# Kernel optimization log

Hardware: AMD Instinct MI355X
Metric: run time of the kernel (lower is better)

The kernel has to match this reference:

```python
import jax, jax.numpy as jnp
import numpy as np

D_MODEL = 1024
N_HEADS = 16
D_K = 64  # per-head dim and the scaling denominator used by the module
NEG = -1e9  # stand-in for -inf in masked_fill (rows are never fully masked)


def setup_inputs() -> dict:
    key = jax.random.key(0)
    ks = jax.random.split(key, 8)
    B, M, N = 2, 2048, 2048
    q = jax.random.normal(ks[0], (B, M, D_MODEL), dtype=jnp.float32)
    k = jax.random.normal(ks[1], (B, N, D_MODEL), dtype=jnp.float32)
    v = jax.random.normal(ks[2], (B, N, D_MODEL), dtype=jnp.float32)
    mask = jax.random.randint(ks[3], (B, M, N), 0, 2).astype(jnp.bool_)
    # xavier_uniform for square [d,d] weights: limit = sqrt(6/(d+d))
    lim = float(np.sqrt(6.0 / (D_MODEL + D_MODEL)))
    Wq = jax.random.uniform(ks[4], (D_MODEL, D_MODEL), jnp.float32, -lim, lim)
    Wk = jax.random.uniform(ks[5], (D_MODEL, D_MODEL), jnp.float32, -lim, lim)
    Wv = jax.random.uniform(ks[6], (D_MODEL, D_MODEL), jnp.float32, -lim, lim)
    Wo = jax.random.uniform(ks[7], (D_MODEL, D_MODEL), jnp.float32, -lim, lim)
    return {"q": q, "k": k, "v": v, "mask": mask,
            "Wq": Wq, "Wk": Wk, "Wv": Wv, "Wo": Wo}


def _split_heads(x):
    # (B, S, D) -> (B, H, S, Dh); the torch split/cat-on-batch trick is
    # mathematically identical to this standard head reshape.
    B, S, _ = x.shape
    return x.reshape(B, S, N_HEADS, D_K).transpose(0, 2, 1, 3)


def reference(q, k, v, mask, Wq, Wk, Wv, Wo):
    qw = _split_heads(q @ Wq.T)  # (B,H,M,Dh)
    kw = _split_heads(k @ Wk.T)  # (B,H,N,Dh)
    vw = _split_heads(v @ Wv.T)  # (B,H,N,Dh)
    scores = jnp.einsum('bhmd,bhnd->bhmn', qw, kw)
    scores = jnp.where(mask[:, None, :, :], NEG, scores)
    attn = jax.nn.softmax(scores / jnp.sqrt(jnp.float32(D_K)), axis=-1)
    ctx = jnp.einsum('bhmn,bhnd->bhmd', attn, vw)
    B, _, M, _ = ctx.shape
    ctx = ctx.transpose(0, 2, 1, 3).reshape(B, M, D_MODEL)
    return ctx @ Wo.T
```

## Files before the change

### kernel.cpp

```cpp
#include <hip/hip_runtime.h>
#include <hip/hip_bf16.h>
#include <stdint.h>
#include <string.h>

#define SEQ   2048
#define DM    1024
#define NH    16
#define NB    2

typedef __attribute__((ext_vector_type(8))) short bf16x8;
typedef __attribute__((ext_vector_type(4))) float f32x4;
typedef unsigned short u16;
typedef unsigned int   u32;

__device__ __forceinline__ u16 f2bf(float f) {
    u32 u = __float_as_uint(f);
    u += 0x7FFF + ((u >> 16) & 1);
    return (u16)(u >> 16);
}
__device__ __forceinline__ u32 pk2bf(float a, float b) {
    __hip_bfloat162 p = __float22bfloat162_rn(make_float2(a, b));
    u32 u; memcpy(&u, &p, 4); return u;
}
__device__ __forceinline__ float fexp2(float x) {
#if __has_builtin(__builtin_amdgcn_exp2f)
    return __builtin_amdgcn_exp2f(x);
#else
    return exp2f(x);
#endif
}
__device__ __forceinline__ float mask_exp2(float s, u32 lsel, int pos) {
#if __has_builtin(__builtin_amdgcn_sbfe)
    u32 keep = (u32)__builtin_amdgcn_sbfe((int)lsel, pos, 1);
#else
    u32 keep = (u32)((int)(lsel << (31 - pos)) >> 31);
#endif
    return __uint_as_float(__float_as_uint(fexp2(s)) & keep);
}
__device__ __forceinline__ void gl_lds16(const void* g, void* l) {
    __builtin_amdgcn_global_load_lds(
        (const __attribute__((address_space(1))) u32*)g,
        (__attribute__((address_space(3))) u32*)l, 16, 0, 0);
}
__device__ __forceinline__ void wbar_vm3() { asm volatile("s_waitcnt vmcnt(3)\ns_barrier" ::: "memory"); }
__device__ __forceinline__ void wbar_vm4() { asm volatile("s_waitcnt vmcnt(4)\ns_barrier" ::: "memory"); }
__device__ __forceinline__ void vm_drain() { asm volatile("s_waitcnt vmcnt(0)" ::: "memory"); }

struct CvtArgs {
    const float* s[7];
    u16* d[7];
    float scale[7];
    int start[8];
};
__global__ __launch_bounds__(256) void cvt_kernel(CvtArgs a) {
    int bid = blockIdx.x;
    int seg = 0;
#pragma unroll
    for (int i = 1; i < 7; ++i) if (bid >= a.start[i]) seg = i;
    float sc = a.scale[seg];
    size_t base = (size_t)(bid - a.start[seg]) * 2048 + threadIdx.x * 8;
    const float4* s4 = (const float4*)(a.s[seg] + base);
    float4 x = s4[0], y = s4[1];
    u32 r[4];
    r[0] = pk2bf(x.x*sc, x.y*sc); r[1] = pk2bf(x.z*sc, x.w*sc);
    r[2] = pk2bf(y.x*sc, y.y*sc); r[3] = pk2bf(y.z*sc, y.w*sc);
    *(uint4*)(a.d[seg] + base) = *(uint4*)r;
}

__global__ void maskpack_kernel(const int* __restrict__ mask,
                                unsigned int* __restrict__ bits) {
    int gid = blockIdx.x * 256 + threadIdx.x;
    int m = mask[gid];
    unsigned long long bal = __ballot(m != 0);
    int lane = threadIdx.x & 63;
    if (lane == 0)       bits[gid >> 5] = (u32)(bal & 0xFFFFFFFFull);
    else if (lane == 32) bits[gid >> 5] = (u32)(bal >> 32);
}

template<int RT>
__device__ __forceinline__ void gemm_body(const u16* __restrict__ A,
                                          const u16* __restrict__ Bm,
                                          void* __restrict__ Y,
                                          int rtile, int ctile, int mode,
                                          u16* sA, u16* sB) {
    constexpr int ABUF = RT * 32 * 32;
    constexpr int BBUF = 128 * 32;
    const int tid  = threadIdx.x;
    const int wv   = tid >> 6, lane = tid & 63;
    const int quad = lane >> 4, ln = lane & 15;
    const int wr   = wv >> 1,  wc  = wv & 1;

    const int lr4 = lane >> 2;
    const int lcc = ((lane & 3) ^ ((lane >> 3) & 3)) * 8;

    const u16* gA[RT/2]; u16* lA[RT/2];
#pragma unroll
    for (int s = 0; s < RT/2; ++s) {
        int seg = wv * (RT/2) + s;
        gA[s] = A + (size_t)(rtile * (RT*32) + seg*16 + lr4) * 1024 + lcc;
        lA[s] = sA + seg * 512;
    }
    const u16* gB[2]; u16* lB[2];
#pragma unroll
    for (int s = 0; s < 2; ++s) {
        int seg = wv * 2 + s;
        gB[s] = Bm + (size_t)(ctile * 128 + seg*16 + lr4) * 1024 + lcc;
        lB[s] = sB + seg * 512;
    }

    f32x4 acc[RT][4];
#pragma unroll
    for (int i = 0; i < RT; ++i)
#pragma unroll
        for (int j = 0; j < 4; ++j) acc[i][j] = (f32x4){0.f,0.f,0.f,0.f};

    const int c0 = (quad ^ ((ln >> 1) & 3)) * 8;

#pragma unroll
    for (int s = 0; s < RT/2; ++s) gl_lds16(gA[s], lA[s]);
#pragma unroll
    for (int s = 0; s < 2; ++s)    gl_lds16(gB[s], lB[s]);
#pragma unroll
    for (int s = 0; s < RT/2; ++s) gl_lds16(gA[s] + 32, lA[s] + ABUF);
#pragma unroll
    for (int s = 0; s < 2; ++s)    gl_lds16(gB[s] + 32, lB[s] + BBUF);

    int bc = 0, bp = 2;
    for (int kt = 0; kt < 32; ++kt) {
        if (RT == 4) wbar_vm4(); else wbar_vm3();
        int pk = (kt + 2) & 31;
#pragma unroll
        for (int s = 0; s < RT/2; ++s) gl_lds16(gA[s] + pk*32, lA[s] + bp*ABUF);
#pragma unroll
        for (int s = 0; s < 2; ++s)    gl_lds16(gB[s] + pk*32, lB[s] + bp*BBUF);

        const u16* sAb = sA + bc * ABUF;
        const u16* sBb = sB + bc * BBUF;
        bf16x8 af[RT], bfr[4];
#pragma unroll
        for (int rt = 0; rt < RT; ++rt)
            af[rt] = *(const bf16x8*)(sAb + (wr*(RT*16) + rt*16 + ln) * 32 + c0);
#pragma unroll
        for (int ct = 0; ct < 4; ++ct)
            bfr[ct] = *(const bf16x8*)(sBb + (wc*64 + ct*16 + ln) * 32 + c0);
#pragma unroll
        for (int rt = 0; rt < RT; ++rt)
#pragma unroll
            for (int ct = 0; ct < 4; ++ct)
                acc[rt][ct] = __builtin_amdgcn_mfma_f32_16x16x32_bf16(
                    af[rt], bfr[ct], acc[rt][ct], 0, 0, 0);

        bc = (bc == 2) ? 0 : bc + 1;
        bp = (bp == 2) ? 0 : bp + 1;
    }
    vm_drain();

#pragma unroll
    for (int rt = 0; rt < RT; ++rt) {
#pragma unroll
        for (int ct = 0; ct < 4; ++ct) {
#pragma unroll
            for (int i = 0; i < 4; ++i) {
                int R = rtile*(RT*32) + wr*(RT*16) + rt*16 + quad*4 + i;
                int C = ctile*128 + wc*64 + ct*16 + ln;
                float val = acc[rt][ct][i];
                if (mode == 0) {
                    int b = R >> 11, s = R & 2047, h = C >> 6, d = C & 63;
                    ((u16*)Y)[((size_t)((b*NH + h) * SEQ + s) << 6) + d] = f2bf(val);
                } else if (mode == 1) {
                    int h = R >> 6, d = R & 63, b = C >> 11, n = C & 2047;
                    ((u16*)Y)[((size_t)((b*NH + h) * 64 + d) << 11) + n] = f2bf(val);
                } else {
                    ((float*)Y)[(size_t)R * 1024 + C] = val;
                }
            }
        }
    }
}

struct QKVArgs { const u16* A[3]; const u16* B[3]; u16* Y[3]; };

__global__ __launch_bounds__(256) void gemm_qkv(QKVArgs g) {
    __shared__ u16 sA[3 * 128 * 32];
    __shared__ u16 sB[3 * 128 * 32];
    int z = blockIdx.z;
    if (z == 2)
        gemm_body<4>(g.A[2], g.B[2], g.Y[2], blockIdx.y, blockIdx.x, 1, sA, sB);
    else
        gemm_body<4>(g.A[z], g.B[z], g.Y[z], blockIdx.x, blockIdx.y, 0, sA, sB);
}

__global__ __launch_bounds__(256) void gemm_out(const u16* __restrict__ A,
                                                const u16* __restrict__ Bm,
                                                float* __restrict__ Y) {
    __shared__ u16 sA[3 * 64 * 32];
    __shared__ u16 sB[3 * 128 * 32];
    gemm_body<2>(A, Bm, Y, blockIdx.x, blockIdx.y, 2, sA, sB);
}

__global__ __launch_bounds__(512) void attn_kernel(
    const u16* __restrict__ qw,
    const u16* __restrict__ kw,
    const u16* __restrict__ vt,
    const u32* __restrict__ mbits,
    u16* __restrict__ ctx) {

    constexpr int RSD = 36;
    __shared__ u16 sK[3 * 4096];
    __shared__ u16 sV[3 * 4096];
    __shared__ u32 sPd[8 * 16 * RSD];

    const int mtile = blockIdx.x;
    const int bh    = blockIdx.y;
    const int b     = bh >> 4;
    const int tid   = threadIdx.x;
    const int wv    = tid >> 6, lane = tid & 63;
    const int quad  = lane >> 4, ln = lane & 15;
    const int m0    = mtile * 128;

    const size_t hbase = (size_t)bh * SEQ * 64;

    bf16x8 qf[2];
    {
        const u16* qp = qw + hbase + (size_t)(m0 + wv*16 + ln) * 64 + quad*8;
        qf[0] = *(const bf16x8*)(qp);
        qf[1] = *(const bf16x8*)(qp + 32);
    }

    f32x4 o[4], lsum;
    lsum = (f32x4){0.f,0.f,0.f,0.f};
#pragma unroll
    for (int j = 0; j < 4; ++j) o[j] = (f32x4){0.f,0.f,0.f,0.f};

    bf16x8 ones;
#pragma unroll
    for (int i = 0; i < 8; ++i) ones[i] = (short)0x3F80;

    const u32* mrow = mbits + (size_t)(b*SEQ + m0 + wv*16 + ln) * 64;

    const int lr = lane >> 3;
    const int lc = (lane & 7) ^ lr;
    const u16* gK = kw + hbase + (size_t)(wv*8 + lr) * 64 + lc*8;
    const u16* gV = vt + hbase + (size_t)(wv*8 + lr) * SEQ + lc*8;
    u16* lK = sK + wv * 512;
    u16* lV = sV + wv * 512;

    const int c0 = (quad ^ (ln & 7)) * 8;
    u32* sPw = sPd + wv * 16 * RSD;
    const u16* sP16 = (const u16*)sPd;

    gl_lds16(gK, lK);
    gl_lds16(gV, lV);
    uint2 wwA = *(const uint2*)(mrow);
    gl_lds16(gK + 4096, lK + 4096);
    gl_lds16(gV + 64,   lV + 4096);
    uint2 wwB = *(const uint2*)(mrow + 2);

    int bc = 0, bp = 2;
    for (int nt = 0; nt < SEQ / 64; ++nt) {
        wbar_vm3();
        int pidx = (nt + 2) & 31;
        gl_lds16(gK + (size_t)pidx * 4096, lK + bp*4096);
        gl_lds16(gV + pidx * 64,           lV + bp*4096);
        uint2 wwC = *(const uint2*)(mrow + pidx*2);

        const u16* sKb = sK + bc * 4096;
        const u16* sVb = sV + bc * 4096;

        f32x4 s4[4];
#pragma unroll
        for (int ct = 0; ct < 4; ++ct) {
            const u16* kp = sKb + (ct*16 + ln) * 64;
            bf16x8 k0 = *(const bf16x8*)(kp + c0);
            bf16x8 k1 = *(const bf16x8*)(kp + (c0 ^ 32));
            f32x4 z = (f32x4){0.f, 0.f, 0.f, 0.f};
            z = __builtin_amdgcn_mfma_f32_16x16x32_bf16(k0, qf[0], z, 0, 0, 0);
            z = __builtin_amdgcn_mfma_f32_16x16x32_bf16(k1, qf[1], z, 0, 0, 0);
            s4[ct] = z;
        }

        {
            u32 l0 = ~(wwA.x >> (quad * 4));
            u32 l1 = ~(wwA.y >> (quad * 4));
#pragma unroll
            for (int ct = 0; ct < 4; ++ct) {
                u32 lsel = (ct & 2) ? l1 : l0;
                float p[4];
#pragma unroll
                for (int i = 0; i < 4; ++i)
                    p[i] = mask_exp2(s4[ct][i], lsel, (ct & 1) * 16 + i);
                uint2 pk;
                pk.x = pk2bf(p[0], p[1]);
                pk.y = pk2bf(p[2], p[3]);
                *(uint2*)(sPw + ln * RSD + ct*8 + quad*2) = pk;
            }
        }

        {
            const u16* pp = sP16 + (wv*16 + ln) * 72;
            bf16x8 pf0 = *(const bf16x8*)(pp + quad*8);
            bf16x8 pf1 = *(const bf16x8*)(pp + 32 + quad*8);
            lsum = __builtin_amdgcn_mfma_f32_16x16x32_bf16(pf0, ones, lsum, 0, 0, 0);
            lsum = __builtin_amdgcn_mfma_f32_16x16x32_bf16(pf1, ones, lsum, 0, 0, 0);
#pragma unroll
            for (int ct = 0; ct < 4; ++ct) {
                const u16* vp = sVb + (ct*16 + ln) * 64;
                bf16x8 v0 = *(const bf16x8*)(vp + c0);
                bf16x8 v1 = *(const bf16x8*)(vp + (c0 ^ 32));
                o[ct] = __builtin_amdgcn_mfma_f32_16x16x32_bf16(pf0, v0, o[ct], 0, 0, 0);
                o[ct] = __builtin_amdgcn_mfma_f32_16x16x32_bf16(pf1, v1, o[ct], 0, 0, 0);
            }
        }

        wwA = wwB;
        wwB = wwC;
        bc = (bc == 2) ? 0 : bc + 1;
        bp = (bp == 2) ? 0 : bp + 1;
    }
    vm_drain();

#pragma unroll
    for (int i = 0; i < 4; ++i) {
        float inv = 1.f / lsum[i];
        int m = m0 + wv*16 + quad*4 + i;
        size_t base = ((size_t)(b * SEQ + m) << 10) + (bh & 15) * 64;
#pragma unroll
        for (int ct = 0; ct < 4; ++ct)
            ctx[base + ct*16 + ln] = f2bf(o[ct][i] * inv);
    }
}

extern "C" void kernel_launch(void* const* d_in, const int* in_sizes, int n_in,
                              void* d_out, int out_size, void* d_ws, size_t ws_size,
                              hipStream_t stream) {
    const float* q    = (const float*)d_in[0];
    const float* k    = (const float*)d_in[1];
    const float* v    = (const float*)d_in[2];
    const int*   mask = (const int*)d_in[3];
    const float* Wq   = (const float*)d_in[4];
    const float* Wk   = (const float*)d_in[5];
    const float* Wv   = (const float*)d_in[6];
    const float* Wo   = (const float*)d_in[7];
    float* out = (float*)d_out;

    char* ws = (char*)d_ws;
    const size_t SZH = (size_t)NB * SEQ * DM * 2;
    const size_t SZW = (size_t)DM * DM * 2;
    u16* qw   = (u16*)(ws);
    u16* kw   = (u16*)(ws + SZH);
    u16* vt   = (u16*)(ws + 2*SZH);
    u16* ctx  = (u16*)(ws + 3*SZH);
    u16* vb   = ctx;
    u32* mbits= (u32*)(ws + 4*SZH);
    u16* qb   = (u16*)(ws + 4*SZH + (1u<<20));
    u16* kb   = (u16*)(ws + 4*SZH + (1u<<20) + SZH);
    u16* Wqb  = (u16*)(ws + 4*SZH + (1u<<20) + 2*SZH);
    u16* Wkb  = (u16*)((char*)Wqb + SZW);
    u16* Wvb  = (u16*)((char*)Wqb + 2*SZW);
    u16* Wob  = (u16*)((char*)Wqb + 3*SZW);

    const float CSC = 0.18033688011112042f;

    CvtArgs ca;
    ca.s[0]=q;  ca.d[0]=qb;  ca.scale[0]=1.f;
    ca.s[1]=k;  ca.d[1]=kb;  ca.scale[1]=1.f;
    ca.s[2]=v;  ca.d[2]=vb;  ca.scale[2]=1.f;
    ca.s[3]=Wq; ca.d[3]=Wqb; ca.scale[3]=CSC;
    ca.s[4]=Wk; ca.d[4]=Wkb; ca.scale[4]=1.f;
    ca.s[5]=Wv; ca.d[5]=Wvb; ca.scale[5]=1.f;
    ca.s[6]=Wo; ca.d[6]=Wob; ca.scale[6]=1.f;
    int st[8] = {0, 2048, 4096, 6144, 6656, 7168, 7680, 8192};
    for (int i = 0; i < 8; ++i) ca.start[i] = st[i];
    cvt_kernel<<<dim3(8192), dim3(256), 0, stream>>>(ca);

    maskpack_kernel<<<dim3(NB*SEQ*SEQ/256), dim3(256), 0, stream>>>(mask, mbits);

    QKVArgs ga;
    ga.A[0]=qb;  ga.B[0]=Wqb; ga.Y[0]=qw;
    ga.A[1]=kb;  ga.B[1]=Wkb; ga.Y[1]=kw;
    ga.A[2]=Wvb; ga.B[2]=vb;  ga.Y[2]=vt;
    gemm_qkv<<<dim3(32, 8, 3), dim3(256), 0, stream>>>(ga);

    attn_kernel<<<dim3(SEQ/128, NB*NH), dim3(512), 0, stream>>>(qw, kw, vt, mbits, ctx);

    gemm_out<<<dim3(64, 8), dim3(256), 0, stream>>>(ctx, Wob, out);
}
```

Baseline: 274.0 us.

## Software-pipeline attention loop: overlap PV of previous tile with QK of current

Restructures the attention main loop so the P·V and row-sum MFMAs for the previous key tile run after the current tile's QK^T MFMAs. P is double-buffered in LDS, K is double-buffered with a one-tile prefetch, and V keeps a three-slot ring with a lagged read index, followed by an epilogue for the last tile. The goal is to hide the exp/pack-to-LDS latency and LDS round trip behind independent matrix work. It also adds launch_bounds occupancy hint 4, which may limit registers, and shortens the K prefetch distance, which could expose global load latency.

New measurement: 265.7 us. 3.0% less time.

```diff
diff --git a/kernel.cpp b/kernel.cpp
--- a/kernel.cpp
+++ b/kernel.cpp
@@ -42,9 +42,11 @@
         (const __attribute__((address_space(1))) u32*)g,
         (__attribute__((address_space(3))) u32*)l, 16, 0, 0);
 }
+__device__ __forceinline__ void wbar_vm2() { asm volatile("s_waitcnt vmcnt(2)\ns_barrier" ::: "memory"); }
 __device__ __forceinline__ void wbar_vm3() { asm volatile("s_waitcnt vmcnt(3)\ns_barrier" ::: "memory"); }
 __device__ __forceinline__ void wbar_vm4() { asm volatile("s_waitcnt vmcnt(4)\ns_barrier" ::: "memory"); }
 __device__ __forceinline__ void vm_drain() { asm volatile("s_waitcnt vmcnt(0)" ::: "memory"); }
+__device__ __forceinline__ void memfence() { asm volatile("" ::: "memory"); }
 
 struct CvtArgs {
     const float* s[7];
@@ -198,17 +200,18 @@
     gemm_body<2>(A, Bm, Y, blockIdx.x, blockIdx.y, 2, sA, sB);
 }
 
-__global__ __launch_bounds__(512) void attn_kernel(
+__global__ __launch_bounds__(512, 4) void attn_kernel(
     const u16* __restrict__ qw,
     const u16* __restrict__ kw,
     const u16* __restrict__ vt,
     const u32* __restrict__ mbits,
     u16* __restrict__ ctx) {
 
-    constexpr int RSD = 36;
-    __shared__ u16 sK[3 * 4096];
+    constexpr int RSD   = 36;
+    constexpr int PSLAB = 8 * 16 * RSD;
+    __shared__ u16 sK[2 * 4096];
     __shared__ u16 sV[3 * 4096];
-    __shared__ u32 sPd[8 * 16 * RSD];
+    __shared__ u32 sPd[2 * PSLAB];
 
     const int mtile = blockIdx.x;
     const int bh    = blockIdx.y;
@@ -246,27 +249,32 @@
     u16* lV = sV + wv * 512;
 
     const int c0 = (quad ^ (ln & 7)) * 8;
-    u32* sPw = sPd + wv * 16 * RSD;
+    u32* sPbase = sPd + wv * 16 * RSD;
     const u16* sP16 = (const u16*)sPd;
 
+    uint2 wwA = *(const uint2*)(mrow);
+    memfence();
     gl_lds16(gK, lK);
+    memfence();
     gl_lds16(gV, lV);
-    uint2 wwA = *(const uint2*)(mrow);
-    gl_lds16(gK + 4096, lK + 4096);
-    gl_lds16(gV + 64,   lV + 4096);
+    memfence();
     uint2 wwB = *(const uint2*)(mrow + 2);
 
-    int bc = 0, bp = 2;
+    int vwb = 1;
+    int vpv = 2;
+
     for (int nt = 0; nt < SEQ / 64; ++nt) {
-        wbar_vm3();
-        int pidx = (nt + 2) & 31;
-        gl_lds16(gK + (size_t)pidx * 4096, lK + bp*4096);
-        gl_lds16(gV + pidx * 64,           lV + bp*4096);
-        uint2 wwC = *(const uint2*)(mrow + pidx*2);
-
-        const u16* sKb = sK + bc * 4096;
-        const u16* sVb = sV + bc * 4096;
-
+        wbar_vm2();
+        const int kc  = nt & 1;
+        const int pkv = (nt + 1) & 31;
+        const int pm  = (nt + 2) & 31;
+        gl_lds16(gK + (size_t)pkv * 4096, lK + (kc ^ 1) * 4096);
+        memfence();
+        gl_lds16(gV + pkv * 64,           lV + vwb * 4096);
+        memfence();
+        uint2 wwC = *(const uint2*)(mrow + pm * 2);
+
+        const u16* sKb = sK + kc * 4096;
         f32x4 s4[4];
 #pragma unroll
         for (int ct = 0; ct < 4; ++ct) {
@@ -279,7 +287,25 @@
             s4[ct] = z;
         }
 
+        if (nt) {
+            const u16* pp  = sP16 + (kc ^ 1) * (PSLAB * 2) + (wv*16 + ln) * 72;
+            const u16* sVb = sV + vpv * 4096;
+            bf16x8 pf0 = *(const bf16x8*)(pp + quad*8);
+            bf16x8 pf1 = *(const bf16x8*)(pp + 32 + quad*8);
+            lsum = __builtin_amdgcn_mfma_f32_16x16x32_bf16(pf0, ones, lsum, 0, 0, 0);
+            lsum = __builtin_amdgcn_mfma_f32_16x16x32_bf16(pf1, ones, lsum, 0, 0, 0);
+#pragma unroll
+            for (int ct = 0; ct < 4; ++ct) {
+                const u16* vp = sVb + (ct*16 + ln) * 64;
+                bf16x8 v0 = *(const bf16x8*)(vp + c0);
+                bf16x8 v1 = *(const bf16x8*)(vp + (c0 ^ 32));
+                o[ct] = __builtin_amdgcn_mfma_f32_16x16x32_bf16(pf0, v0, o[ct], 0, 0, 0);
+                o[ct] = __builtin_amdgcn_mfma_f32_16x16x32_bf16(pf1, v1, o[ct], 0, 0, 0);
+            }
+        }
+
         {
+            u32* sPw = sPbase + kc * PSLAB;
             u32 l0 = ~(wwA.x >> (quad * 4));
             u32 l1 = ~(wwA.y >> (quad * 4));
 #pragma unroll
@@ -296,28 +322,28 @@
             }
         }
 
-        {
-            const u16* pp = sP16 + (wv*16 + ln) * 72;
-            bf16x8 pf0 = *(const bf16x8*)(pp + quad*8);
-            bf16x8 pf1 = *(const bf16x8*)(pp + 32 + quad*8);
-            lsum = __builtin_amdgcn_mfma_f32_16x16x32_bf16(pf0, ones, lsum, 0, 0, 0);
-            lsum = __builtin_amdgcn_mfma_f32_16x16x32_bf16(pf1, ones, lsum, 0, 0, 0);
-#pragma unroll
-            for (int ct = 0; ct < 4; ++ct) {
-                const u16* vp = sVb + (ct*16 + ln) * 64;
-                bf16x8 v0 = *(const bf16x8*)(vp + c0);
-                bf16x8 v1 = *(const bf16x8*)(vp + (c0 ^ 32));
-                o[ct] = __builtin_amdgcn_mfma_f32_16x16x32_bf16(pf0, v0, o[ct], 0, 0, 0);
-                o[ct] = __builtin_amdgcn_mfma_f32_16x16x32_bf16(pf1, v1, o[ct], 0, 0, 0);
-            }
+        wwA = wwB; wwB = wwC;
+        vwb = (vwb == 2) ? 0 : vwb + 1;
+        vpv = (vpv == 2) ? 0 : vpv + 1;
+    }
+    vm_drain();
+
+    {
+        const u16* pp  = sP16 + 1 * (PSLAB * 2) + (wv*16 + ln) * 72;
+        const u16* sVb = sV + 1 * 4096;
+        bf16x8 pf0 = *(const bf16x8*)(pp + quad*8);
+        bf16x8 pf1 = *(const bf16x8*)(pp + 32 + quad*8);
+        lsum = __builtin_amdgcn_mfma_f32_16x16x32_bf16(pf0, ones, lsum, 0, 0, 0);
+        lsum = __builtin_amdgcn_mfma_f32_16x16x32_bf16(pf1, ones, lsum, 0, 0, 0);
+#pragma unroll
+        for (int ct = 0; ct < 4; ++ct) {
+            const u16* vp = sVb + (ct*16 + ln) * 64;
+            bf16x8 v0 = *(const bf16x8*)(vp + c0);
+            bf16x8 v1 = *(const bf16x8*)(vp + (c0 ^ 32));
+            o[ct] = __builtin_amdgcn_mfma_f32_16x16x32_bf16(pf0, v0, o[ct], 0, 0, 0);
+            o[ct] = __builtin_amdgcn_mfma_f32_16x16x32_bf16(pf1, v1, o[ct], 0, 0, 0);
         }
-
-        wwA = wwB;
-        wwB = wwC;
-        bc = (bc == 2) ? 0 : bc + 1;
-        bp = (bp == 2) ? 0 : bp + 1;
-    }
-    vm_drain();
+    }
 
 #pragma unroll
     for (int i = 0; i < 4; ++i) {
```

## Keep attention probabilities in registers instead of round-tripping through LDS

Applied to the files above, without the earlier changes.

The softmax probabilities are now packed straight into MFMA A-operand registers, and the V operand is gathered with a k-index permutation that matches the register layout the score MFMA produces. This removes the per-tile LDS write and read of P, and the sPd shared buffer. A launch-bounds occupancy hint is added. V reads become four 8-byte loads per tile instead of two 16-byte loads, so LDS instruction count rises.

Measured after the change: 266.4 us. -2.8%, faster.

```diff
diff --git a/kernel.cpp b/kernel.cpp
--- a/kernel.cpp
+++ b/kernel.cpp
@@ -198,17 +198,15 @@
     gemm_body<2>(A, Bm, Y, blockIdx.x, blockIdx.y, 2, sA, sB);
 }
 
-__global__ __launch_bounds__(512) void attn_kernel(
+__global__ __launch_bounds__(512, 6) void attn_kernel(
     const u16* __restrict__ qw,
     const u16* __restrict__ kw,
     const u16* __restrict__ vt,
     const u32* __restrict__ mbits,
     u16* __restrict__ ctx) {
 
-    constexpr int RSD = 36;
     __shared__ u16 sK[3 * 4096];
     __shared__ u16 sV[3 * 4096];
-    __shared__ u32 sPd[8 * 16 * RSD];
 
     const int mtile = blockIdx.x;
     const int bh    = blockIdx.y;
@@ -246,8 +244,12 @@
     u16* lV = sV + wv * 512;
 
     const int c0 = (quad ^ (ln & 7)) * 8;
-    u32* sPw = sPd + wv * 16 * RSD;
-    const u16* sP16 = (const u16*)sPd;
+
+    const int qh = quad >> 1, h4 = (quad & 1) * 4, sw = ln & 7;
+    const int cA0 = ((qh    ) ^ sw) * 8 + h4;
+    const int cA1 = ((qh + 2) ^ sw) * 8 + h4;
+    const int cB0 = ((qh + 4) ^ sw) * 8 + h4;
+    const int cB1 = ((qh + 6) ^ sw) * 8 + h4;
 
     gl_lds16(gK, lK);
     gl_lds16(gV, lV);
@@ -279,6 +281,7 @@
             s4[ct] = z;
         }
 
+        u32 P0[4], P1[4];
         {
             u32 l0 = ~(wwA.x >> (quad * 4));
             u32 l1 = ~(wwA.y >> (quad * 4));
@@ -289,31 +292,37 @@
 #pragma unroll
                 for (int i = 0; i < 4; ++i)
                     p[i] = mask_exp2(s4[ct][i], lsel, (ct & 1) * 16 + i);
-                uint2 pk;
-                pk.x = pk2bf(p[0], p[1]);
-                pk.y = pk2bf(p[2], p[3]);
-                *(uint2*)(sPw + ln * RSD + ct*8 + quad*2) = pk;
+                u32 lo = pk2bf(p[0], p[1]);
+                u32 hi = pk2bf(p[2], p[3]);
+                if (ct == 0)      { P0[0] = lo; P0[1] = hi; }
+                else if (ct == 1) { P0[2] = lo; P0[3] = hi; }
+                else if (ct == 2) { P1[0] = lo; P1[1] = hi; }
+                else              { P1[2] = lo; P1[3] = hi; }
             }
         }
-
-        {
-            const u16* pp = sP16 + (wv*16 + ln) * 72;
-            bf16x8 pf0 = *(const bf16x8*)(pp + quad*8);
-            bf16x8 pf1 = *(const bf16x8*)(pp + 32 + quad*8);
-            lsum = __builtin_amdgcn_mfma_f32_16x16x32_bf16(pf0, ones, lsum, 0, 0, 0);
-            lsum = __builtin_amdgcn_mfma_f32_16x16x32_bf16(pf1, ones, lsum, 0, 0, 0);
-#pragma unroll
-            for (int ct = 0; ct < 4; ++ct) {
-                const u16* vp = sVb + (ct*16 + ln) * 64;
-                bf16x8 v0 = *(const bf16x8*)(vp + c0);
-                bf16x8 v1 = *(const bf16x8*)(vp + (c0 ^ 32));
-                o[ct] = __builtin_amdgcn_mfma_f32_16x16x32_bf16(pf0, v0, o[ct], 0, 0, 0);
-                o[ct] = __builtin_amdgcn_mfma_f32_16x16x32_bf16(pf1, v1, o[ct], 0, 0, 0);
-            }
+        bf16x8 pf0, pf1;
+        memcpy(&pf0, P0, 16);
+        memcpy(&pf1, P1, 16);
+
+        lsum = __builtin_amdgcn_mfma_f32_16x16x32_bf16(pf0, ones, lsum, 0, 0, 0);
+        lsum = __builtin_amdgcn_mfma_f32_16x16x32_bf16(pf1, ones, lsum, 0, 0, 0);
+#pragma unroll
+        for (int ct = 0; ct < 4; ++ct) {
+            const u16* vrow = sVb + (ct*16 + ln) * 64;
+            uint2 a0 = *(const uint2*)(vrow + cA0);
+            uint2 a1 = *(const uint2*)(vrow + cA1);
+            uint2 b0 = *(const uint2*)(vrow + cB0);
+            uint2 b1 = *(const uint2*)(vrow + cB1);
+            u32 V0[4] = {a0.x, a0.y, a1.x, a1.y};
+            u32 V1[4] = {b0.x, b0.y, b1.x, b1.y};
+            bf16x8 vf0, vf1;
+            memcpy(&vf0, V0, 16);
+            memcpy(&vf1, V1, 16);
+            o[ct] = __builtin_amdgcn_mfma_f32_16x16x32_bf16(pf0, vf0, o[ct], 0, 0, 0);
+            o[ct] = __builtin_amdgcn_mfma_f32_16x16x32_bf16(pf1, vf1, o[ct], 0, 0, 0);
         }
 
-        wwA = wwB;
-        wwB = wwC;
+        wwA = wwB; wwB = wwC;
         bc = (bc == 2) ? 0 : bc + 1;
         bp = (bp == 2) ? 0 : bp + 1;
     }
```
